# Kernel tuning notes

Hardware: AMD Instinct MI355X
Metric: run time of the kernel (lower is better)

Reference implementation:

```python
import jax, jax.numpy as jnp
import numpy as np

HEADS = 16
ROPE_BASE = 10000.0


def _apply_rope(x, shift=0):
    # x: [b, h, s, d]; pairs (2i, 2i+1) form complex numbers rotated by m*theta_i
    b, h, s, d = x.shape
    half = d // 2
    theta = jnp.exp(-jnp.log(ROPE_BASE) * jnp.arange(0, d, 2, dtype=jnp.float32) / d)  # [half]
    m = jnp.arange(shift, shift + s, dtype=jnp.float32)[:, None]                        # [s,1]
    freqs = m * theta[None, :]                                                          # [s,half]
    cos = jnp.cos(freqs)[None, None]                                                    # [1,1,s,half]
    sin = jnp.sin(freqs)[None, None]
    xr = x.reshape(b, h, s, half, 2)
    xe, xo = xr[..., 0], xr[..., 1]
    oe = xe * cos - xo * sin
    oo = xe * sin + xo * cos
    return jnp.stack([oe, oo], axis=-1).reshape(b, h, s, d)


def setup_inputs() -> dict:
    key = jax.random.key(0)
    ks = jax.random.split(key, 4)
    b, s, dim = 2, 2048, 2048
    x = jax.random.normal(ks[0], (b, s, dim), dtype=jnp.float32)
    Wq = jax.random.normal(ks[1], (dim, dim), dtype=jnp.float32) * 0.02
    Wk = jax.random.normal(ks[2], (dim, dim), dtype=jnp.float32) * 0.02
    Wv = jax.random.normal(ks[3], (dim, dim), dtype=jnp.float32) * 0.02
    return {"x": x, "Wq": Wq, "Wk": Wk, "Wv": Wv}


def reference(x, Wq, Wk, Wv):
    b, s, dim = x.shape
    h = HEADS
    d = dim // h
    # QKV projections (torch Linear: y = x @ W^T), split into heads: b h s d
    q = jnp.einsum('bsm,nm->bsn', x, Wq).reshape(b, s, h, d).transpose(0, 2, 1, 3)
    k = jnp.einsum('bsm,nm->bsn', x, Wk).reshape(b, s, h, d).transpose(0, 2, 1, 3)
    v = jnp.einsum('bsm,nm->bsn', x, Wv).reshape(b, s, h, d).transpose(0, 2, 1, 3)
    # RoPE (torch version is under no_grad -> detached)
    q = jax.lax.stop_gradient(_apply_rope(q.astype(jnp.float32)))
    k = jax.lax.stop_gradient(_apply_rope(k.astype(jnp.float32)))
    # causal scaled dot-product attention, fp32 softmax
    scale = 1.0 / jnp.sqrt(jnp.float32(d))
    scores = jnp.einsum('bhqd,bhkd->bhqk', q, k).astype(jnp.float32) * scale
    causal = jnp.tril(jnp.ones((s, s), dtype=bool))
    scores = jnp.where(causal[None, None], scores, jnp.float32(-1e30))
    attn = jax.nn.softmax(scores, axis=-1)
    out = jnp.einsum('bhqk,bhkd->bhqd', attn, v.astype(jnp.float32))
    # b h s d -> b s (h d)
    return out.transpose(0, 2, 1, 3).reshape(b, s, dim)
```

## Files before the change

### kernel.cpp

```cpp
#include <hip/hip_runtime.h>
#include <hip/hip_bf16.h>
#include <stdint.h>

typedef __bf16 bf16;
typedef bf16 bf16x8 __attribute__((ext_vector_type(8)));
typedef bf16 bf16x4 __attribute__((ext_vector_type(4)));
typedef float f32x4 __attribute__((ext_vector_type(4)));

#define MFMA16(a, b, c) __builtin_amdgcn_mfma_f32_16x16x32_bf16(a, b, c, 0, 0, 0)

static __device__ __forceinline__ bf16 f2b(float f) { return (bf16)f; }
static __device__ __forceinline__ float b2f(bf16 v) { return (float)v; }

static __device__ __forceinline__ void gload16(const void* src, void* dst) {
    __builtin_amdgcn_global_load_lds(
        (const __attribute__((address_space(1))) uint32_t*)src,
        (__attribute__((address_space(3))) uint32_t*)dst, 16, 0, 0);
}

static __device__ __forceinline__ uint32_t cvtpk(float lo, float hi) {
    uint32_t r;
    asm volatile("v_cvt_pk_bf16_f32 %0, %1, %2" : "=v"(r) : "v"(lo), "v"(hi));
    return r;
}

__global__ void cvt_all(const float* __restrict__ x,  const float* __restrict__ wq,
                        const float* __restrict__ wk, const float* __restrict__ wv,
                        bf16* __restrict__ xb,  bf16* __restrict__ wqb,
                        bf16* __restrict__ wkb, bf16* __restrict__ wvb) {
    int i = blockIdx.x * blockDim.x + threadIdx.x;
    const float* src; bf16* dst; int off;
    if (i < 2097152)      { src = x;  dst = xb;  off = i; }
    else if (i < 3145728) { src = wq; dst = wqb; off = i - 2097152; }
    else if (i < 4194304) { src = wk; dst = wkb; off = i - 3145728; }
    else                  { src = wv; dst = wvb; off = i - 4194304; }
    float4 v = reinterpret_cast<const float4*>(src)[off];
    bf16x4 o;
    o[0] = f2b(v.x); o[1] = f2b(v.y); o[2] = f2b(v.z); o[3] = f2b(v.w);
    reinterpret_cast<bf16x4*>(dst)[off] = o;
}

__global__ void rope_table(float2* __restrict__ tbl) {
    int t = blockIdx.x * blockDim.x + threadIdx.x;
    int i = t & 63;
    int s = t >> 6;
    float theta = expf(-9.210340371976184f * (float)(2 * i) * (1.0f / 128.0f));
    float freq = (float)s * theta;
    float sv, cv;
    sincosf(freq, &sv, &cv);
    tbl[t] = make_float2(cv, sv);
}

__global__ __launch_bounds__(256) void gemm_qkv(const bf16* __restrict__ X,
                                                const bf16* __restrict__ Wq,
                                                const bf16* __restrict__ Wk,
                                                const bf16* __restrict__ Wv,
                                                bf16* __restrict__ Qm,
                                                bf16* __restrict__ Km,
                                                bf16* __restrict__ Vt,
                                                const float2* __restrict__ tbl) {
    const int K = 2048;
    __shared__ bf16 As[2][128 * 64];
    __shared__ bf16 Bs[2][128 * 64];

    const int z = blockIdx.z;
    const bf16* W = (z == 0) ? Wq : (z == 1) ? Wk : Wv;

    const int tid  = threadIdx.x;
    const int lane = tid & 63;
    const int w    = tid >> 6;
    const int wr   = (w >> 1) * 64;
    const int wc   = (w & 1) * 64;
    const int l15  = lane & 15;
    const int l4   = lane >> 4;
    const int rbase = blockIdx.x * 128;
    const int cbase = blockIdx.y * 128;

    const int srow  = lane >> 3;
    const int sslot = lane & 7;

    f32x4 acc[4][4] = {};

    auto stage = [&](int buf, int kt) {
#pragma unroll
        for (int i = 0; i < 4; ++i) {
            int c   = w * 4 + i;
            int row = c * 8 + srow;
            int gsl = sslot ^ (row & 7);
            gload16(&X[(size_t)(rbase + row) * K + kt + gsl * 8], (char*)As[buf] + c * 1024);
            gload16(&W[(size_t)(cbase + row) * K + kt + gsl * 8], (char*)Bs[buf] + c * 1024);
        }
    };

    stage(0, 0);
    __syncthreads();
    int cur = 0;

    for (int kt = 0; kt < K; kt += 64) {
        if (kt + 64 < K) stage(cur ^ 1, kt + 64);

        bf16x8 af[2][4], bfr[2][4];
#pragma unroll
        for (int ks = 0; ks < 2; ++ks) {
#pragma unroll
            for (int mi = 0; mi < 4; ++mi) {
                int r    = wr + mi * 16 + l15;
                int phys = (ks * 4 + l4) ^ (r & 7);
                af[ks][mi] = *reinterpret_cast<const bf16x8*>(
                    (char*)As[cur] + r * 128 + phys * 16);
            }
#pragma unroll
            for (int ni = 0; ni < 4; ++ni) {
                int r    = wc + ni * 16 + l15;
                int phys = (ks * 4 + l4) ^ (r & 7);
                bfr[ks][ni] = *reinterpret_cast<const bf16x8*>(
                    (char*)Bs[cur] + r * 128 + phys * 16);
            }
        }
#pragma unroll
        for (int ks = 0; ks < 2; ++ks)
#pragma unroll
            for (int mi = 0; mi < 4; ++mi)
#pragma unroll
                for (int ni = 0; ni < 4; ++ni)
                    acc[mi][ni] = MFMA16(af[ks][mi], bfr[ks][ni], acc[mi][ni]);

        __syncthreads();
        cur ^= 1;
    }

    if (z < 2) {
        bf16* Y = (z == 0) ? Qm : Km;
        const float scale = (z == 0) ? 0.1275174396094198f : 1.0f;
        const int odd = l15 & 1;
#pragma unroll
        for (int mi = 0; mi < 4; ++mi) {
            int r0 = rbase + wr + mi * 16 + l4 * 4;
#pragma unroll
            for (int i = 0; i < 4; ++i) {
                int r = r0 + i;
                int b = r >> 11, s = r & 2047;
#pragma unroll
                for (int ni = 0; ni < 4; ++ni) {
                    int n = cbase + wc + ni * 16 + l15;
                    int h = n >> 7, d = n & 127;
                    float v = acc[mi][ni][i];
                    float p = __shfl_xor(v, 1);
                    float2 cs = tbl[(s << 6) + (d >> 1)];
                    float res = v * cs.x + (odd ? p : -p) * cs.y;
                    Y[(((size_t)b * 16 + h) * 2048 + s) * 128 + d] = f2b(res * scale);
                }
            }
        }
    } else {
#pragma unroll
        for (int mi = 0; mi < 4; ++mi) {
            int r0 = rbase + wr + mi * 16 + l4 * 4;
            int b = r0 >> 11, s = r0 & 2047;
#pragma unroll
            for (int ni = 0; ni < 4; ++ni) {
                int n = cbase + wc + ni * 16 + l15;
                int h = n >> 7, d = n & 127;
                bf16x4 o;
#pragma unroll
                for (int i = 0; i < 4; ++i) o[i] = f2b(acc[mi][ni][i]);
                *reinterpret_cast<bf16x4*>(&Vt[(((size_t)b * 16 + h) * 128 + d) * 2048 + s]) = o;
            }
        }
    }
}

__global__ __launch_bounds__(256, 4) void flash_attn(const bf16* __restrict__ Q,
                                                     const bf16* __restrict__ Km,
                                                     const bf16* __restrict__ Vt,
                                                     float* __restrict__ out) {
    __shared__ bf16 Ksh[64 * 128];
    __shared__ bf16 Vsh[128 * 64];

    const int tid  = threadIdx.x;
    const int lane = tid & 63;
    const int w    = tid >> 6;
    const int l15  = lane & 15;
    const int l4   = lane >> 4;

    const int bx  = blockIdx.x;
    const int g   = (bx >> 5) & 7;
    const int seg = bx >> 8;
    const int qt  = (seg == 0) ? 31 - g : (seg == 1) ? g : (seg == 2) ? 23 - g : 8 + g;
    const int bh  = bx & 31;
    const int b   = bh >> 4, h = bh & 15;

    const bf16* Qb = Q  + (size_t)bh * 2048 * 128;
    const bf16* Kb = Km + (size_t)bh * 2048 * 128;
    const bf16* Vb = Vt + (size_t)bh * 128 * 2048;
    const int rw = qt * 64 + w * 16;

    auto stage = [&](int kvb) {
#pragma unroll
        for (int c4 = 0; c4 < 4; ++c4) {
            int c  = w * 4 + c4;
            int kr = c * 4 + (lane >> 4);
            int ks = (lane & 15) ^ (kr & 7);
            gload16((const char*)Kb + ((size_t)(kvb + kr) * 128 + ks * 8) * 2,
                    (char*)Ksh + c * 1024);
            int vr = c * 8 + (lane >> 3);
            int vs = (lane & 7) ^ (vr & 7);
            gload16((const char*)Vb + ((size_t)vr * 2048 + kvb + vs * 8) * 2,
                    (char*)Vsh + c * 1024);
        }
    };

    bf16x8 qf[4];
#pragma unroll
    for (int ks = 0; ks < 4; ++ks)
        qf[ks] = *reinterpret_cast<const bf16x8*>(
            &Qb[(size_t)(rw + l15) * 128 + ks * 32 + l4 * 8]);

    f32x4 o[8] = {};
    float mrow = -1e30f, lrow = 0.0f;

    const int xbase = l15 + ((lane >> 4) & 1) * 32;
    const bool hiL  = (lane >> 5) & 1;

    for (int t = 0; t <= qt; ++t) {
        const int kvb = t * 64;
        __syncthreads();
        stage(kvb);
        __syncthreads();

        const char* kb = (const char*)Ksh;
        f32x4 s4[4] = {};
        __builtin_amdgcn_s_setprio(1);
#pragma unroll
        for (int t4 = 0; t4 < 4; ++t4) {
            int r = t4 * 16 + l15;
#pragma unroll
            for (int ks = 0; ks < 4; ++ks) {
                int phys = (ks * 4 + l4) ^ (r & 7);
                bf16x8 kf = *reinterpret_cast<const bf16x8*>(kb + r * 256 + phys * 16);
                s4[t4] = MFMA16(kf, qf[ks], s4[t4]);
            }
        }
        __builtin_amdgcn_s_setprio(0);

        if (t == qt) {
            int q = rw + l15;
#pragma unroll
            for (int t4 = 0; t4 < 4; ++t4)
#pragma unroll
                for (int i = 0; i < 4; ++i)
                    if (kvb + t4 * 16 + l4 * 4 + i > q) s4[t4][i] = -1e30f;
        }

        float sm = -1e30f;
#pragma unroll
        for (int t4 = 0; t4 < 4; ++t4)
#pragma unroll
            for (int i = 0; i < 4; ++i) sm = fmaxf(sm, s4[t4][i]);
        sm = fmaxf(sm, __shfl_xor(sm, 16));
        sm = fmaxf(sm, __shfl_xor(sm, 32));
        float nm    = fmaxf(mrow, sm);
        float alpha = __builtin_amdgcn_exp2f(mrow - nm);
        mrow = nm;
        float ps = 0.0f;
#pragma unroll
        for (int t4 = 0; t4 < 4; ++t4)
#pragma unroll
            for (int i = 0; i < 4; ++i) {
                float p = __builtin_amdgcn_exp2f(s4[t4][i] - nm);
                s4[t4][i] = p;
                ps += p;
            }
        ps += __shfl_xor(ps, 16);
        ps += __shfl_xor(ps, 32);
        lrow = lrow * alpha + ps;

        float ai[4];
#pragma unroll
        for (int i = 0; i < 4; ++i)
            ai[i] = __shfl(alpha, (lane & 48) + l4 * 4 + i);
#pragma unroll
        for (int ds = 0; ds < 8; ++ds)
#pragma unroll
            for (int i = 0; i < 4; ++i) o[ds][i] *= ai[i];

        uint32_t own[8];
#pragma unroll
        for (int t4 = 0; t4 < 4; ++t4) {
            own[t4 * 2 + 0] = cvtpk(s4[t4][0], s4[t4][1]);
            own[t4 * 2 + 1] = cvtpk(s4[t4][2], s4[t4][3]);
        }
        bf16x8 pa[2];
#pragma unroll
        for (int ks2 = 0; ks2 < 2; ++ks2) {
            union { uint32_t u[4]; bf16x8 v; } pu;
#pragma unroll
            for (int s = 0; s < 4; ++s) {
                int srcl = xbase + 16 * (s >> 1);
                uint32_t ulo = (uint32_t)__shfl((int)own[ks2 * 4 + (s & 1)], srcl);
                uint32_t uhi = (uint32_t)__shfl((int)own[ks2 * 4 + 2 + (s & 1)], srcl);
                pu.u[s] = hiL ? uhi : ulo;
            }
            pa[ks2] = pu.v;
        }

        const char* vb = (const char*)Vsh;
        __builtin_amdgcn_s_setprio(1);
#pragma unroll
        for (int k2 = 0; k2 < 2; ++k2) {
#pragma unroll
            for (int ds = 0; ds < 8; ++ds) {
                int d     = ds * 16 + l15;
                int physv = (k2 * 4 + l4) ^ (d & 7);
                bf16x8 vf = *reinterpret_cast<const bf16x8*>(vb + d * 128 + physv * 16);
                o[ds] = MFMA16(pa[k2], vf, o[ds]);
            }
        }
        __builtin_amdgcn_s_setprio(0);
    }

    float inv = 1.0f / lrow;
    float iv[4];
#pragma unroll
    for (int i = 0; i < 4; ++i)
        iv[i] = __shfl(inv, (lane & 48) + l4 * 4 + i);
#pragma unroll
    for (int i = 0; i < 4; ++i) {
        int row = rw + l4 * 4 + i;
#pragma unroll
        for (int ds = 0; ds < 8; ++ds)
            out[((size_t)b * 2048 + row) * 2048 + h * 128 + ds * 16 + l15] =
                o[ds][i] * iv[i];
    }
}

extern "C" void kernel_launch(void* const* d_in, const int* in_sizes, int n_in,
                              void* d_out, int out_size, void* d_ws, size_t ws_size,
                              hipStream_t stream) {
    const float* x  = (const float*)d_in[0];
    const float* Wq = (const float*)d_in[1];
    const float* Wk = (const float*)d_in[2];
    const float* Wv = (const float*)d_in[3];
    float* out = (float*)d_out;
    char* ws = (char*)d_ws;

    bf16* xb   = (bf16*)(ws + 0);
    bf16* wqb  = (bf16*)(ws + 16777216);
    bf16* wkb  = (bf16*)(ws + 25165824);
    bf16* wvb  = (bf16*)(ws + 33554432);
    bf16* Qm   = (bf16*)(ws + 41943040);
    bf16* Km   = (bf16*)(ws + 58720256);
    bf16* Vt   = (bf16*)(ws + 75497472);
    float2* tbl = (float2*)(ws + 92274688);

    cvt_all<<<20480, 256, 0, stream>>>(x, Wq, Wk, Wv, xb, wqb, wkb, wvb);
    rope_table<<<512, 256, 0, stream>>>(tbl);

    dim3 gg(32, 16, 3);
    gemm_qkv<<<gg, 256, 0, stream>>>(xb, wqb, wkb, wvb, Qm, Km, Vt, tbl);

    flash_attn<<<1024, 256, 0, stream>>>(Qm, Km, Vt, out);
}
```

Before: 216.2 us.

## Enlarge QKV GEMM tiles to 256x256 with 512 threads and XCD-aware block remap

The QKV projection GEMM moves from 128x128 tiles with 4 waves to 256x256 tiles with 8 waves. Each wave now computes a 128x64 sub-tile and reuses its B fragments across two halves of A. The 3D grid becomes a flat 384-block grid, and block ids are remapped so neighbouring tiles land on the same XCD. This is meant to cut global and L2 traffic per FLOP. The cost is 128KB of LDS per block, one block per CU, and a 1.5-wave tail across the CUs.

After: 228.5 us. +5.7%, slower.

```diff
diff --git a/kernel.cpp b/kernel.cpp
--- a/kernel.cpp
+++ b/kernel.cpp
@@ -51,35 +51,36 @@
     tbl[t] = make_float2(cv, sv);
 }
 
-__global__ __launch_bounds__(256) void gemm_qkv(const bf16* __restrict__ X,
-                                                const bf16* __restrict__ Wq,
-                                                const bf16* __restrict__ Wk,
-                                                const bf16* __restrict__ Wv,
-                                                bf16* __restrict__ Qm,
-                                                bf16* __restrict__ Km,
-                                                bf16* __restrict__ Vt,
-                                                const float2* __restrict__ tbl) {
+__global__ __launch_bounds__(512, 1) void gemm_qkv(const bf16* __restrict__ X,
+                                                   const bf16* __restrict__ Wq,
+                                                   const bf16* __restrict__ Wk,
+                                                   const bf16* __restrict__ Wv,
+                                                   bf16* __restrict__ Qm,
+                                                   bf16* __restrict__ Km,
+                                                   bf16* __restrict__ Vt,
+                                                   const float2* __restrict__ tbl) {
     const int K = 2048;
-    __shared__ bf16 As[2][128 * 64];
-    __shared__ bf16 Bs[2][128 * 64];
-
-    const int z = blockIdx.z;
+    __shared__ bf16 As[2][256 * 64];
+    __shared__ bf16 Bs[2][256 * 64];
+
+    const int bid = blockIdx.x;
+    const int wg  = (bid & 7) * 48 + (bid >> 3);
+    const int z   = wg >> 7;
+    const int t   = wg & 127;
+    const int rbase = (t >> 3) * 256;
+    const int cbase = (t & 7) * 256;
+
     const bf16* W = (z == 0) ? Wq : (z == 1) ? Wk : Wv;
 
     const int tid  = threadIdx.x;
     const int lane = tid & 63;
     const int w    = tid >> 6;
-    const int wr   = (w >> 1) * 64;
-    const int wc   = (w & 1) * 64;
+    const int wm   = w >> 2;
+    const int wn   = w & 3;
     const int l15  = lane & 15;
     const int l4   = lane >> 4;
-    const int rbase = blockIdx.x * 128;
-    const int cbase = blockIdx.y * 128;
-
     const int srow  = lane >> 3;
     const int sslot = lane & 7;
-
-    f32x4 acc[4][4] = {};
 
     auto stage = [&](int buf, int kt) {
 #pragma unroll
@@ -91,6 +92,18 @@
             gload16(&W[(size_t)(cbase + row) * K + kt + gsl * 8], (char*)Bs[buf] + c * 1024);
         }
     };
+    auto rdA = [&](int buf, int mi, int ks) {
+        int r    = wm * 128 + mi * 16 + l15;
+        int phys = (ks * 4 + l4) ^ (r & 7);
+        return *reinterpret_cast<const bf16x8*>((char*)As[buf] + r * 128 + phys * 16);
+    };
+    auto rdB = [&](int buf, int ni, int ks) {
+        int r    = wn * 64 + ni * 16 + l15;
+        int phys = (ks * 4 + l4) ^ (r & 7);
+        return *reinterpret_cast<const bf16x8*>((char*)Bs[buf] + r * 128 + phys * 16);
+    };
+
+    f32x4 acc[8][4] = {};
 
     stage(0, 0);
     __syncthreads();
@@ -99,31 +112,42 @@
     for (int kt = 0; kt < K; kt += 64) {
         if (kt + 64 < K) stage(cur ^ 1, kt + 64);
 
-        bf16x8 af[2][4], bfr[2][4];
-#pragma unroll
-        for (int ks = 0; ks < 2; ++ks) {
+        bf16x8 bfr[4][2];
+#pragma unroll
+        for (int ni = 0; ni < 4; ++ni) {
+            bfr[ni][0] = rdB(cur, ni, 0);
+            bfr[ni][1] = rdB(cur, ni, 1);
+        }
+        {
+            bf16x8 af[4][2];
 #pragma unroll
             for (int mi = 0; mi < 4; ++mi) {
-                int r    = wr + mi * 16 + l15;
-                int phys = (ks * 4 + l4) ^ (r & 7);
-                af[ks][mi] = *reinterpret_cast<const bf16x8*>(
-                    (char*)As[cur] + r * 128 + phys * 16);
-            }
-#pragma unroll
-            for (int ni = 0; ni < 4; ++ni) {
-                int r    = wc + ni * 16 + l15;
-                int phys = (ks * 4 + l4) ^ (r & 7);
-                bfr[ks][ni] = *reinterpret_cast<const bf16x8*>(
-                    (char*)Bs[cur] + r * 128 + phys * 16);
-            }
-        }
-#pragma unroll
-        for (int ks = 0; ks < 2; ++ks)
-#pragma unroll
-            for (int mi = 0; mi < 4; ++mi)
-#pragma unroll
-                for (int ni = 0; ni < 4; ++ni)
-                    acc[mi][ni] = MFMA16(af[ks][mi], bfr[ks][ni], acc[mi][ni]);
+                af[mi][0] = rdA(cur, mi, 0);
+                af[mi][1] = rdA(cur, mi, 1);
+            }
+#pragma unroll
+            for (int ks = 0; ks < 2; ++ks)
+#pragma unroll
+                for (int mi = 0; mi < 4; ++mi)
+#pragma unroll
+                    for (int ni = 0; ni < 4; ++ni)
+                        acc[mi][ni] = MFMA16(af[mi][ks], bfr[ni][ks], acc[mi][ni]);
+        }
+        {
+            bf16x8 af[4][2];
+#pragma unroll
+            for (int mi = 0; mi < 4; ++mi) {
+                af[mi][0] = rdA(cur, mi + 4, 0);
+                af[mi][1] = rdA(cur, mi + 4, 1);
+            }
+#pragma unroll
+            for (int ks = 0; ks < 2; ++ks)
+#pragma unroll
+                for (int mi = 0; mi < 4; ++mi)
+#pragma unroll
+                    for (int ni = 0; ni < 4; ++ni)
+                        acc[mi + 4][ni] = MFMA16(af[mi][ks], bfr[ni][ks], acc[mi + 4][ni]);
+        }
 
         __syncthreads();
         cur ^= 1;
@@ -134,15 +158,15 @@
         const float scale = (z == 0) ? 0.1275174396094198f : 1.0f;
         const int odd = l15 & 1;
 #pragma unroll
-        for (int mi = 0; mi < 4; ++mi) {
-            int r0 = rbase + wr + mi * 16 + l4 * 4;
+        for (int mi = 0; mi < 8; ++mi) {
+            int r0 = rbase + wm * 128 + mi * 16 + l4 * 4;
 #pragma unroll
             for (int i = 0; i < 4; ++i) {
                 int r = r0 + i;
                 int b = r >> 11, s = r & 2047;
 #pragma unroll
                 for (int ni = 0; ni < 4; ++ni) {
-                    int n = cbase + wc + ni * 16 + l15;
+                    int n = cbase + wn * 64 + ni * 16 + l15;
                     int h = n >> 7, d = n & 127;
                     float v = acc[mi][ni][i];
                     float p = __shfl_xor(v, 1);
@@ -154,12 +178,12 @@
         }
     } else {
 #pragma unroll
-        for (int mi = 0; mi < 4; ++mi) {
-            int r0 = rbase + wr + mi * 16 + l4 * 4;
+        for (int mi = 0; mi < 8; ++mi) {
+            int r0 = rbase + wm * 128 + mi * 16 + l4 * 4;
             int b = r0 >> 11, s = r0 & 2047;
 #pragma unroll
             for (int ni = 0; ni < 4; ++ni) {
-                int n = cbase + wc + ni * 16 + l15;
+                int n = cbase + wn * 64 + ni * 16 + l15;
                 int h = n >> 7, d = n & 127;
                 bf16x4 o;
 #pragma unroll
@@ -356,8 +380,7 @@
     cvt_all<<<20480, 256, 0, stream>>>(x, Wq, Wk, Wv, xb, wqb, wkb, wvb);
     rope_table<<<512, 256, 0, stream>>>(tbl);
 
-    dim3 gg(32, 16, 3);
-    gemm_qkv<<<gg, 256, 0, stream>>>(xb, wqb, wkb, wvb, Qm, Km, Vt, tbl);
+    gemm_qkv<<<384, 512, 0, stream>>>(xb, wqb, wkb, wvb, Qm, Km, Vt, tbl);
 
     flash_attn<<<1024, 256, 0, stream>>>(Qm, Km, Vt, out);
 }
```

## Double query rows per attention block and fold rope table into convert kernel

Applied to the files above, without the earlier changes.

Each flash-attention block now covers 128 query rows: every wave handles two 16-row query tiles against each staged K/V tile, halving the grid and reusing every K/V fragment read from shared memory for two MFMAs. Query tiles are paired (qt and 23-qt style) to balance causal work, and waves skip KV tiles that lie fully beyond their rows. Launch bounds drop to 2 blocks per SM to allow the larger register footprint. The rope table computation is merged into the conversion kernel, removing one launch. Risks are lower occupancy, more register pressure, and fewer blocks (512) for load balancing.

After: 218.0 us. No clear change (+0.9%).

```diff
diff --git a/kernel.cpp b/kernel.cpp
--- a/kernel.cpp
+++ b/kernel.cpp
@@ -27,7 +27,18 @@
 __global__ void cvt_all(const float* __restrict__ x,  const float* __restrict__ wq,
                         const float* __restrict__ wk, const float* __restrict__ wv,
                         bf16* __restrict__ xb,  bf16* __restrict__ wqb,
-                        bf16* __restrict__ wkb, bf16* __restrict__ wvb) {
+                        bf16* __restrict__ wkb, bf16* __restrict__ wvb,
+                        float2* __restrict__ tbl) {
+    if (blockIdx.x >= 20480) {
+        int t = (blockIdx.x - 20480) * blockDim.x + threadIdx.x;
+        int i = t & 63;
+        int s = t >> 6;
+        float theta = expf(-9.210340371976184f * (float)(2 * i) * (1.0f / 128.0f));
+        float sv, cv;
+        sincosf((float)s * theta, &sv, &cv);
+        tbl[t] = make_float2(cv, sv);
+        return;
+    }
     int i = blockIdx.x * blockDim.x + threadIdx.x;
     const float* src; bf16* dst; int off;
     if (i < 2097152)      { src = x;  dst = xb;  off = i; }
@@ -38,17 +49,6 @@
     bf16x4 o;
     o[0] = f2b(v.x); o[1] = f2b(v.y); o[2] = f2b(v.z); o[3] = f2b(v.w);
     reinterpret_cast<bf16x4*>(dst)[off] = o;
-}
-
-__global__ void rope_table(float2* __restrict__ tbl) {
-    int t = blockIdx.x * blockDim.x + threadIdx.x;
-    int i = t & 63;
-    int s = t >> 6;
-    float theta = expf(-9.210340371976184f * (float)(2 * i) * (1.0f / 128.0f));
-    float freq = (float)s * theta;
-    float sv, cv;
-    sincosf(freq, &sv, &cv);
-    tbl[t] = make_float2(cv, sv);
 }
 
 __global__ __launch_bounds__(256) void gemm_qkv(const bf16* __restrict__ X,
@@ -170,7 +170,7 @@
     }
 }
 
-__global__ __launch_bounds__(256, 4) void flash_attn(const bf16* __restrict__ Q,
+__global__ __launch_bounds__(256, 2) void flash_attn(const bf16* __restrict__ Q,
                                                      const bf16* __restrict__ Km,
                                                      const bf16* __restrict__ Vt,
                                                      float* __restrict__ out) {
@@ -183,17 +183,15 @@
     const int l15  = lane & 15;
     const int l4   = lane >> 4;
 
-    const int bx  = blockIdx.x;
-    const int g   = (bx >> 5) & 7;
-    const int seg = bx >> 8;
-    const int qt  = (seg == 0) ? 31 - g : (seg == 1) ? g : (seg == 2) ? 23 - g : 8 + g;
-    const int bh  = bx & 31;
-    const int b   = bh >> 4, h = bh & 15;
+    const int bx = blockIdx.x;
+    const int bh = bx & 31;
+    const int qt = (bx < 256) ? (bx >> 5) : 23 - (bx >> 5);
+    const int b  = bh >> 4, h = bh & 15;
 
     const bf16* Qb = Q  + (size_t)bh * 2048 * 128;
     const bf16* Kb = Km + (size_t)bh * 2048 * 128;
     const bf16* Vb = Vt + (size_t)bh * 128 * 2048;
-    const int rw = qt * 64 + w * 16;
+    const int rw = qt * 128 + w * 32;
 
     auto stage = [&](int kvb) {
 #pragma unroll
@@ -210,26 +208,31 @@
         }
     };
 
-    bf16x8 qf[4];
-#pragma unroll
-    for (int ks = 0; ks < 4; ++ks)
-        qf[ks] = *reinterpret_cast<const bf16x8*>(
-            &Qb[(size_t)(rw + l15) * 128 + ks * 32 + l4 * 8]);
-
-    f32x4 o[8] = {};
-    float mrow = -1e30f, lrow = 0.0f;
-
-    const int xbase = l15 + ((lane >> 4) & 1) * 32;
-    const bool hiL  = (lane >> 5) & 1;
-
-    for (int t = 0; t <= qt; ++t) {
+    bf16x8 qf[2][4];
+#pragma unroll
+    for (int qi = 0; qi < 2; ++qi)
+#pragma unroll
+        for (int ks = 0; ks < 4; ++ks)
+            qf[qi][ks] = *reinterpret_cast<const bf16x8*>(
+                &Qb[(size_t)(rw + qi * 16 + l15) * 128 + ks * 32 + l4 * 8]);
+
+    f32x4 o[2][8] = {};
+    float mrow[2] = {-1e30f, -1e30f}, lrow[2] = {0.0f, 0.0f};
+
+    const int xbase = l15 + (l4 & 1) * 32;
+    const bool hiL  = (l4 >> 1) & 1;
+
+    const int n = 2 * qt + 2;
+    for (int t = 0; t < n; ++t) {
         const int kvb = t * 64;
         __syncthreads();
         stage(kvb);
         __syncthreads();
 
+        if (kvb > rw + 31) continue;
+
         const char* kb = (const char*)Ksh;
-        f32x4 s4[4] = {};
+        f32x4 s4[2][4] = {};
         __builtin_amdgcn_s_setprio(1);
 #pragma unroll
         for (int t4 = 0; t4 < 4; ++t4) {
@@ -238,70 +241,77 @@
             for (int ks = 0; ks < 4; ++ks) {
                 int phys = (ks * 4 + l4) ^ (r & 7);
                 bf16x8 kf = *reinterpret_cast<const bf16x8*>(kb + r * 256 + phys * 16);
-                s4[t4] = MFMA16(kf, qf[ks], s4[t4]);
+                s4[0][t4] = MFMA16(kf, qf[0][ks], s4[0][t4]);
+                s4[1][t4] = MFMA16(kf, qf[1][ks], s4[1][t4]);
             }
         }
         __builtin_amdgcn_s_setprio(0);
 
-        if (t == qt) {
-            int q = rw + l15;
+        if (kvb + 63 > rw) {
+#pragma unroll
+            for (int qi = 0; qi < 2; ++qi) {
+                int q = rw + qi * 16 + l15;
+#pragma unroll
+                for (int t4 = 0; t4 < 4; ++t4)
+#pragma unroll
+                    for (int i = 0; i < 4; ++i)
+                        if (kvb + t4 * 16 + l4 * 4 + i > q) s4[qi][t4][i] = -1e30f;
+            }
+        }
+
+        bf16x8 pa[2][2];
+#pragma unroll
+        for (int qi = 0; qi < 2; ++qi) {
+            float sm = -1e30f;
 #pragma unroll
             for (int t4 = 0; t4 < 4; ++t4)
 #pragma unroll
-                for (int i = 0; i < 4; ++i)
-                    if (kvb + t4 * 16 + l4 * 4 + i > q) s4[t4][i] = -1e30f;
-        }
-
-        float sm = -1e30f;
-#pragma unroll
-        for (int t4 = 0; t4 < 4; ++t4)
-#pragma unroll
-            for (int i = 0; i < 4; ++i) sm = fmaxf(sm, s4[t4][i]);
-        sm = fmaxf(sm, __shfl_xor(sm, 16));
-        sm = fmaxf(sm, __shfl_xor(sm, 32));
-        float nm    = fmaxf(mrow, sm);
-        float alpha = __builtin_amdgcn_exp2f(mrow - nm);
-        mrow = nm;
-        float ps = 0.0f;
-#pragma unroll
-        for (int t4 = 0; t4 < 4; ++t4)
-#pragma unroll
-            for (int i = 0; i < 4; ++i) {
-                float p = __builtin_amdgcn_exp2f(s4[t4][i] - nm);
-                s4[t4][i] = p;
-                ps += p;
-            }
-        ps += __shfl_xor(ps, 16);
-        ps += __shfl_xor(ps, 32);
-        lrow = lrow * alpha + ps;
-
-        float ai[4];
-#pragma unroll
-        for (int i = 0; i < 4; ++i)
-            ai[i] = __shfl(alpha, (lane & 48) + l4 * 4 + i);
-#pragma unroll
-        for (int ds = 0; ds < 8; ++ds)
-#pragma unroll
-            for (int i = 0; i < 4; ++i) o[ds][i] *= ai[i];
-
-        uint32_t own[8];
-#pragma unroll
-        for (int t4 = 0; t4 < 4; ++t4) {
-            own[t4 * 2 + 0] = cvtpk(s4[t4][0], s4[t4][1]);
-            own[t4 * 2 + 1] = cvtpk(s4[t4][2], s4[t4][3]);
-        }
-        bf16x8 pa[2];
-#pragma unroll
-        for (int ks2 = 0; ks2 < 2; ++ks2) {
-            union { uint32_t u[4]; bf16x8 v; } pu;
-#pragma unroll
-            for (int s = 0; s < 4; ++s) {
-                int srcl = xbase + 16 * (s >> 1);
-                uint32_t ulo = (uint32_t)__shfl((int)own[ks2 * 4 + (s & 1)], srcl);
-                uint32_t uhi = (uint32_t)__shfl((int)own[ks2 * 4 + 2 + (s & 1)], srcl);
-                pu.u[s] = hiL ? uhi : ulo;
-            }
-            pa[ks2] = pu.v;
+                for (int i = 0; i < 4; ++i) sm = fmaxf(sm, s4[qi][t4][i]);
+            sm = fmaxf(sm, __shfl_xor(sm, 16));
+            sm = fmaxf(sm, __shfl_xor(sm, 32));
+            float nm    = fmaxf(mrow[qi], sm);
+            float alpha = __builtin_amdgcn_exp2f(mrow[qi] - nm);
+            mrow[qi] = nm;
+            float ps = 0.0f;
+#pragma unroll
+            for (int t4 = 0; t4 < 4; ++t4)
+#pragma unroll
+                for (int i = 0; i < 4; ++i) {
+                    float p = __builtin_amdgcn_exp2f(s4[qi][t4][i] - nm);
+                    s4[qi][t4][i] = p;
+                    ps += p;
+                }
+            ps += __shfl_xor(ps, 16);
+            ps += __shfl_xor(ps, 32);
+            lrow[qi] = lrow[qi] * alpha + ps;
+
+            float ai[4];
+#pragma unroll
+            for (int i = 0; i < 4; ++i)
+                ai[i] = __shfl(alpha, (lane & 48) + l4 * 4 + i);
+#pragma unroll
+            for (int ds = 0; ds < 8; ++ds)
+#pragma unroll
+                for (int i = 0; i < 4; ++i) o[qi][ds][i] *= ai[i];
+
+            uint32_t own[8];
+#pragma unroll
+            for (int t4 = 0; t4 < 4; ++t4) {
+                own[t4 * 2 + 0] = cvtpk(s4[qi][t4][0], s4[qi][t4][1]);
+                own[t4 * 2 + 1] = cvtpk(s4[qi][t4][2], s4[qi][t4][3]);
+            }
+#pragma unroll
+            for (int ks2 = 0; ks2 < 2; ++ks2) {
+                union { uint32_t u[4]; bf16x8 v; } pu;
+#pragma unroll
+                for (int s = 0; s < 4; ++s) {
+                    int srcl = xbase + 16 * (s >> 1);
+                    uint32_t ulo = (uint32_t)__shfl((int)own[ks2 * 4 + (s & 1)], srcl);
+                    uint32_t uhi = (uint32_t)__shfl((int)own[ks2 * 4 + 2 + (s & 1)], srcl);
+                    pu.u[s] = hiL ? uhi : ulo;
+                }
+                pa[qi][ks2] = pu.v;
+            }
         }
 
         const char* vb = (const char*)Vsh;
@@ -313,24 +323,28 @@
                 int d     = ds * 16 + l15;
                 int physv = (k2 * 4 + l4) ^ (d & 7);
                 bf16x8 vf = *reinterpret_cast<const bf16x8*>(vb + d * 128 + physv * 16);
-                o[ds] = MFMA16(pa[k2], vf, o[ds]);
+                o[0][ds] = MFMA16(pa[0][k2], vf, o[0][ds]);
+                o[1][ds] = MFMA16(pa[1][k2], vf, o[1][ds]);
             }
         }
         __builtin_amdgcn_s_setprio(0);
     }
 
-    float inv = 1.0f / lrow;
-    float iv[4];
-#pragma unroll
-    for (int i = 0; i < 4; ++i)
-        iv[i] = __shfl(inv, (lane & 48) + l4 * 4 + i);
-#pragma unroll
-    for (int i = 0; i < 4; ++i) {
-        int row = rw + l4 * 4 + i;
-#pragma unroll
-        for (int ds = 0; ds < 8; ++ds)
-            out[((size_t)b * 2048 + row) * 2048 + h * 128 + ds * 16 + l15] =
-                o[ds][i] * iv[i];
+#pragma unroll
+    for (int qi = 0; qi < 2; ++qi) {
+        float inv = 1.0f / lrow[qi];
+        float iv[4];
+#pragma unroll
+        for (int i = 0; i < 4; ++i)
+            iv[i] = __shfl(inv, (lane & 48) + l4 * 4 + i);
+#pragma unroll
+        for (int i = 0; i < 4; ++i) {
+            int row = rw + qi * 16 + l4 * 4 + i;
+#pragma unroll
+            for (int ds = 0; ds < 8; ++ds)
+                out[((size_t)b * 2048 + row) * 2048 + h * 128 + ds * 16 + l15] =
+                    o[qi][ds][i] * iv[i];
+        }
     }
 }
 
@@ -353,11 +367,10 @@
     bf16* Vt   = (bf16*)(ws + 75497472);
     float2* tbl = (float2*)(ws + 92274688);
 
-    cvt_all<<<20480, 256, 0, stream>>>(x, Wq, Wk, Wv, xb, wqb, wkb, wvb);
-    rope_table<<<512, 256, 0, stream>>>(tbl);
+    cvt_all<<<20992, 256, 0, stream>>>(x, Wq, Wk, Wv, xb, wqb, wkb, wvb, tbl);
 
     dim3 gg(32, 16, 3);
     gemm_qkv<<<gg, 256, 0, stream>>>(xb, wqb, wkb, wvb, Qm, Km, Vt, tbl);
 
-    flash_attn<<<1024, 256, 0, stream>>>(Qm, Km, Vt, out);
-}
+    flash_attn<<<512, 256, 0, stream>>>(Qm, Km, Vt, out);
+}
```
